# Kernel tuning notes

Hardware: AMD Instinct MI355X
Metric: run time of the kernel (lower is better)

The kernel has to match this reference:

```python
import jax, jax.numpy as jnp
import numpy as np

IN = 1    # input feature dim (hardcoded in NN)
H = 10    # LSTM hidden size (hardcoded in NN)
B = 8192  # batch
T = 256   # sequence length


def setup_inputs() -> dict:
    key = jax.random.key(0)
    ks = jax.random.split(key, 12)
    s = 0.1  # init scale for mus (mimics blitz posterior_mu_init spread)
    RHO0 = -3.0  # posterior_rho_init from the module
    return {
        "x": jax.random.normal(ks[0], (B, T, IN), jnp.float32),
        # BayesianLSTM variational parameters (blitz layout: (in, 4*H), (H, 4*H), (4*H,))
        "w_ih_mu": jax.random.normal(ks[1], (IN, 4 * H), jnp.float32) * s,
        "w_ih_rho": jnp.full((IN, 4 * H), RHO0, jnp.float32),
        "w_hh_mu": jax.random.normal(ks[2], (H, 4 * H), jnp.float32) * s,
        "w_hh_rho": jnp.full((H, 4 * H), RHO0, jnp.float32),
        "b_mu": jax.random.normal(ks[3], (4 * H,), jnp.float32) * s,
        "b_rho": jnp.full((4 * H,), RHO0, jnp.float32),
        # reparameterization noise, sampled once per forward call in blitz
        "eps_ih": jax.random.normal(ks[4], (IN, 4 * H), jnp.float32),
        "eps_hh": jax.random.normal(ks[5], (H, 4 * H), jnp.float32),
        "eps_b": jax.random.normal(ks[6], (4 * H,), jnp.float32),
        # deterministic linear head nn.Linear(10, 1)
        "lin_w": jax.random.normal(ks[7], (1, H), jnp.float32) * s,
        "lin_b": jnp.zeros((1,), jnp.float32),
    }


def reference(x, w_ih_mu, w_ih_rho, w_hh_mu, w_hh_rho, b_mu, b_rho,
              eps_ih, eps_hh, eps_b, lin_w, lin_b):
    sp = jax.nn.softplus
    # sample weights: w = mu + log1p(exp(rho)) * eps
    w_ih = w_ih_mu + sp(w_ih_rho) * eps_ih   # (IN, 4H)
    w_hh = w_hh_mu + sp(w_hh_rho) * eps_hh   # (H, 4H)
    b = b_mu + sp(b_rho) * eps_b             # (4H,)

    # precompute input contribution for all timesteps: (B, T, 4H)
    x_proj = jnp.einsum('bti,ig->btg', x, w_ih) + b

    def step(carry, xg):
        h, c = carry                      # (B, H) each
        gates = xg + h @ w_hh             # (B, 4H)
        i = jax.nn.sigmoid(gates[:, :H])
        f = jax.nn.sigmoid(gates[:, H:2 * H])
        g = jnp.tanh(gates[:, 2 * H:3 * H])
        o = jax.nn.sigmoid(gates[:, 3 * H:])
        c = f * c + i * g
        h = o * jnp.tanh(c)
        return (h, c), None

    h0 = jnp.zeros((x.shape[0], H), x.dtype)
    (h_last, _), _ = jax.lax.scan(step, (h0, h0), jnp.swapaxes(x_proj, 0, 1))
    # NN takes hidden_seq[:, -1, :] == final hidden state, then linear head
    return h_last @ lin_w.T + lin_b  # (B, 1)
```

## Files before the change

kernel.cpp:

```cpp
#include <hip/hip_runtime.h>
#include <math.h>

#define T_LEN 256
#define HID 10

typedef float v2f __attribute__((ext_vector_type(2)));

__device__ __forceinline__ v2f mk2(float a, float b) { v2f r; r.x = a; r.y = b; return r; }
__device__ __forceinline__ v2f splat2(float a) { return mk2(a, a); }

__device__ __forceinline__ float softplus_f(float x) {
    return fmaxf(x, 0.0f) + log1pf(expf(-fabsf(x)));
}
__device__ __forceinline__ float samp(const float* mu, const float* rho,
                                      const float* eps, int i) {
    return mu[i] + softplus_f(rho[i]) * eps[i];
}

__device__ __forceinline__ float fast_sigmoid(float x) {
    float e = __builtin_amdgcn_exp2f(-1.442695040888963f * x);
    return __builtin_amdgcn_rcpf(1.0f + e);
}
__device__ __forceinline__ float fast_tanh(float x) {
    float e = __builtin_amdgcn_exp2f(2.885390081777927f * x);
    return fmaf(-2.0f, __builtin_amdgcn_rcpf(e + 1.0f), 1.0f);
}

#define ROTF(hi, R) __int_as_float(__builtin_amdgcn_mov_dpp((hi), 0x120 + (R), 0xF, 0xF, true))

struct Wreg {
    v2f wsel01[16], wsel23[16];
    v2f wih01, wih23, b01, b23;
};

__device__ __forceinline__ float lstm_step(const Wreg& w, float xt, float hk,
                                           float& c)
{
    const int hi = __float_as_int(hk);
    v2f x2 = splat2(xt);
    v2f e01 = __builtin_elementwise_fma(x2, w.wih01, w.b01);
    v2f e23 = __builtin_elementwise_fma(x2, w.wih23, w.b23);
    v2f o01 = w.wsel01[0] * splat2(hk);
    v2f o23 = w.wsel23[0] * splat2(hk);
#define RSTEP(R, A01, A23)                                            \
    {                                                                 \
        v2f hr = splat2(ROTF(hi, R));                                 \
        A01 = __builtin_elementwise_fma(hr, w.wsel01[R], A01);        \
        A23 = __builtin_elementwise_fma(hr, w.wsel23[R], A23);        \
    }
    RSTEP(1,  e01, e23)
    RSTEP(2,  o01, o23)
    RSTEP(3,  e01, e23)
    RSTEP(4,  o01, o23)
    RSTEP(5,  e01, e23)
    RSTEP(6,  o01, o23)
    RSTEP(7,  e01, e23)
    RSTEP(8,  o01, o23)
    RSTEP(9,  e01, e23)
    RSTEP(10, o01, o23)
    RSTEP(11, e01, e23)
    RSTEP(12, o01, o23)
    RSTEP(13, e01, e23)
    RSTEP(14, o01, o23)
    RSTEP(15, e01, e23)
#undef RSTEP
    v2f a01 = e01 + o01;
    v2f a23 = e23 + o23;
    float ig = fast_sigmoid(a01.x);
    float fg = fast_sigmoid(a01.y);
    float gg = fast_tanh(a23.x);
    float og = fast_sigmoid(a23.y);
    c = fmaf(fg, c, ig * gg);
    return og * fast_tanh(c);
}

__global__ __launch_bounds__(64) void bayes_lstm_kernel(
    const float* __restrict__ x,
    const float* __restrict__ w_ih_mu, const float* __restrict__ w_ih_rho,
    const float* __restrict__ w_hh_mu, const float* __restrict__ w_hh_rho,
    const float* __restrict__ b_mu,    const float* __restrict__ b_rho,
    const float* __restrict__ eps_ih,  const float* __restrict__ eps_hh,
    const float* __restrict__ eps_b,
    const float* __restrict__ lin_w,   const float* __restrict__ lin_b,
    float* __restrict__ out, int n_elem)
{
    const int lane = threadIdx.x & 63;
    const int k    = lane & 15;
    const int g    = lane >> 4;
    const int b    = blockIdx.x * 4 + g;
    const int b_eff = (b < n_elem) ? b : (n_elem - 1);
    const bool un  = (k < HID);

    Wreg w;
    w.wih01 = splat2(0.f); w.wih23 = splat2(0.f);
    w.b01 = splat2(0.f);   w.b23 = splat2(0.f);
    if (un) {
        const int c0 = k, c1 = HID + k, c2 = 2 * HID + k, c3 = 3 * HID + k;
        w.wih01 = mk2(samp(w_ih_mu, w_ih_rho, eps_ih, c0), samp(w_ih_mu, w_ih_rho, eps_ih, c1));
        w.wih23 = mk2(samp(w_ih_mu, w_ih_rho, eps_ih, c2), samp(w_ih_mu, w_ih_rho, eps_ih, c3));
        w.b01   = mk2(samp(b_mu, b_rho, eps_b, c0), samp(b_mu, b_rho, eps_b, c1));
        w.b23   = mk2(samp(b_mu, b_rho, eps_b, c2), samp(b_mu, b_rho, eps_b, c3));
    }
#pragma unroll
    for (int r = 0; r < 16; ++r) {
        const int idx = (k - r) & 15;
        if (un && idx < HID) {
            const int base = idx * 4 * HID;
            w.wsel01[r] = mk2(samp(w_hh_mu, w_hh_rho, eps_hh, base + k),
                              samp(w_hh_mu, w_hh_rho, eps_hh, base + HID + k));
            w.wsel23[r] = mk2(samp(w_hh_mu, w_hh_rho, eps_hh, base + 2 * HID + k),
                              samp(w_hh_mu, w_hh_rho, eps_hh, base + 3 * HID + k));
        } else {
            w.wsel01[r] = splat2(0.f);
            w.wsel23[r] = splat2(0.f);
        }
    }

    float c = 0.f, hk = 0.f;
    const float4* xv = (const float4*)(x + (size_t)b_eff * T_LEN);
    float4 xq = xv[0];
    for (int ch = 0; ch < 64; ++ch) {
        const int nx = (ch < 63) ? ch + 1 : 63;
        float4 xn = xv[nx];
        hk = lstm_step(w, xq.x, hk, c);
        hk = lstm_step(w, xq.y, hk, c);
        hk = lstm_step(w, xq.z, hk, c);
        hk = lstm_step(w, xq.w, hk, c);
        xq = xn;
    }

    const float lw = un ? lin_w[k] : 0.f;
    float pa = hk * lw;
    pa += __shfl_xor(pa, 1, 16);
    pa += __shfl_xor(pa, 2, 16);
    pa += __shfl_xor(pa, 4, 16);
    pa += __shfl_xor(pa, 8, 16);
    if (k == 0 && b < n_elem) out[b] = pa + lin_b[0];
}

extern "C" void kernel_launch(void* const* d_in, const int* in_sizes, int n_in,
                              void* d_out, int out_size, void* d_ws, size_t ws_size,
                              hipStream_t stream) {
    const float* x        = (const float*)d_in[0];
    const float* w_ih_mu  = (const float*)d_in[1];
    const float* w_ih_rho = (const float*)d_in[2];
    const float* w_hh_mu  = (const float*)d_in[3];
    const float* w_hh_rho = (const float*)d_in[4];
    const float* b_mu     = (const float*)d_in[5];
    const float* b_rho    = (const float*)d_in[6];
    const float* eps_ih   = (const float*)d_in[7];
    const float* eps_hh   = (const float*)d_in[8];
    const float* eps_b    = (const float*)d_in[9];
    const float* lin_w    = (const float*)d_in[10];
    const float* lin_b    = (const float*)d_in[11];
    float* out = (float*)d_out;

    const int n_b = in_sizes[0] / T_LEN;
    dim3 grid((n_b + 3) / 4), block(64);
    hipLaunchKernelGGL(bayes_lstm_kernel, grid, block, 0, stream,
                       x, w_ih_mu, w_ih_rho, w_hh_mu, w_hh_rho, b_mu, b_rho,
                       eps_ih, eps_hh, eps_b, lin_w, lin_b, out, n_b);
}
```

Before: 188.1 us.

## Interleave two batch sequences per lane group and fold activation scales into weights

```diff
diff --git a/kernel.cpp b/kernel.cpp
--- a/kernel.cpp
+++ b/kernel.cpp
@@ -17,12 +17,17 @@
     return mu[i] + softplus_f(rho[i]) * eps[i];
 }
 
-__device__ __forceinline__ float fast_sigmoid(float x) {
-    float e = __builtin_amdgcn_exp2f(-1.442695040888963f * x);
-    return __builtin_amdgcn_rcpf(1.0f + e);
+#define NLOG2E (-1.442695040888963f)
+#define P2LOG2E (2.885390081777927f)
+
+__device__ __forceinline__ float sig_pre(float a) {
+    return __builtin_amdgcn_rcpf(1.0f + __builtin_amdgcn_exp2f(a));
+}
+__device__ __forceinline__ float tanh_pre(float a) {
+    return fmaf(-2.0f, __builtin_amdgcn_rcpf(__builtin_amdgcn_exp2f(a) + 1.0f), 1.0f);
 }
 __device__ __forceinline__ float fast_tanh(float x) {
-    float e = __builtin_amdgcn_exp2f(2.885390081777927f * x);
+    float e = __builtin_amdgcn_exp2f(P2LOG2E * x);
     return fmaf(-2.0f, __builtin_amdgcn_rcpf(e + 1.0f), 1.0f);
 }
 
@@ -66,10 +71,10 @@
 #undef RSTEP
     v2f a01 = e01 + o01;
     v2f a23 = e23 + o23;
-    float ig = fast_sigmoid(a01.x);
-    float fg = fast_sigmoid(a01.y);
-    float gg = fast_tanh(a23.x);
-    float og = fast_sigmoid(a23.y);
+    float ig = sig_pre(a01.x);
+    float fg = sig_pre(a01.y);
+    float gg = tanh_pre(a23.x);
+    float og = sig_pre(a23.y);
     c = fmaf(fg, c, ig * gg);
     return og * fast_tanh(c);
 }
@@ -86,56 +91,71 @@
 {
     const int lane = threadIdx.x & 63;
     const int k    = lane & 15;
-    const int g    = lane >> 4;
-    const int b    = blockIdx.x * 4 + g;
-    const int b_eff = (b < n_elem) ? b : (n_elem - 1);
+    const int row  = lane >> 4;
+    const int bA   = blockIdx.x * 8 + row * 2;
+    const int bB   = bA + 1;
+    const int bAe  = (bA < n_elem) ? bA : (n_elem - 1);
+    const int bBe  = (bB < n_elem) ? bB : (n_elem - 1);
     const bool un  = (k < HID);
 
     Wreg w;
     w.wih01 = splat2(0.f); w.wih23 = splat2(0.f);
     w.b01 = splat2(0.f);   w.b23 = splat2(0.f);
+    const v2f s01 = mk2(NLOG2E, NLOG2E);
+    const v2f s23 = mk2(P2LOG2E, NLOG2E);
     if (un) {
         const int c0 = k, c1 = HID + k, c2 = 2 * HID + k, c3 = 3 * HID + k;
-        w.wih01 = mk2(samp(w_ih_mu, w_ih_rho, eps_ih, c0), samp(w_ih_mu, w_ih_rho, eps_ih, c1));
-        w.wih23 = mk2(samp(w_ih_mu, w_ih_rho, eps_ih, c2), samp(w_ih_mu, w_ih_rho, eps_ih, c3));
-        w.b01   = mk2(samp(b_mu, b_rho, eps_b, c0), samp(b_mu, b_rho, eps_b, c1));
-        w.b23   = mk2(samp(b_mu, b_rho, eps_b, c2), samp(b_mu, b_rho, eps_b, c3));
+        w.wih01 = s01 * mk2(samp(w_ih_mu, w_ih_rho, eps_ih, c0), samp(w_ih_mu, w_ih_rho, eps_ih, c1));
+        w.wih23 = s23 * mk2(samp(w_ih_mu, w_ih_rho, eps_ih, c2), samp(w_ih_mu, w_ih_rho, eps_ih, c3));
+        w.b01   = s01 * mk2(samp(b_mu, b_rho, eps_b, c0), samp(b_mu, b_rho, eps_b, c1));
+        w.b23   = s23 * mk2(samp(b_mu, b_rho, eps_b, c2), samp(b_mu, b_rho, eps_b, c3));
     }
 #pragma unroll
     for (int r = 0; r < 16; ++r) {
         const int idx = (k - r) & 15;
         if (un && idx < HID) {
             const int base = idx * 4 * HID;
-            w.wsel01[r] = mk2(samp(w_hh_mu, w_hh_rho, eps_hh, base + k),
-                              samp(w_hh_mu, w_hh_rho, eps_hh, base + HID + k));
-            w.wsel23[r] = mk2(samp(w_hh_mu, w_hh_rho, eps_hh, base + 2 * HID + k),
-                              samp(w_hh_mu, w_hh_rho, eps_hh, base + 3 * HID + k));
+            w.wsel01[r] = s01 * mk2(samp(w_hh_mu, w_hh_rho, eps_hh, base + k),
+                                    samp(w_hh_mu, w_hh_rho, eps_hh, base + HID + k));
+            w.wsel23[r] = s23 * mk2(samp(w_hh_mu, w_hh_rho, eps_hh, base + 2 * HID + k),
+                                    samp(w_hh_mu, w_hh_rho, eps_hh, base + 3 * HID + k));
         } else {
             w.wsel01[r] = splat2(0.f);
             w.wsel23[r] = splat2(0.f);
         }
     }
 
-    float c = 0.f, hk = 0.f;
-    const float4* xv = (const float4*)(x + (size_t)b_eff * T_LEN);
-    float4 xq = xv[0];
+    float cA = 0.f, hkA = 0.f, cB = 0.f, hkB = 0.f;
+    const float4* xvA = (const float4*)(x + (size_t)bAe * T_LEN);
+    const float4* xvB = (const float4*)(x + (size_t)bBe * T_LEN);
+    float4 xqA = xvA[0], xqB = xvB[0];
     for (int ch = 0; ch < 64; ++ch) {
         const int nx = (ch < 63) ? ch + 1 : 63;
-        float4 xn = xv[nx];
-        hk = lstm_step(w, xq.x, hk, c);
-        hk = lstm_step(w, xq.y, hk, c);
-        hk = lstm_step(w, xq.z, hk, c);
-        hk = lstm_step(w, xq.w, hk, c);
-        xq = xn;
+        float4 xnA = xvA[nx];
+        float4 xnB = xvB[nx];
+        hkA = lstm_step(w, xqA.x, hkA, cA);
+        hkB = lstm_step(w, xqB.x, hkB, cB);
+        hkA = lstm_step(w, xqA.y, hkA, cA);
+        hkB = lstm_step(w, xqB.y, hkB, cB);
+        hkA = lstm_step(w, xqA.z, hkA, cA);
+        hkB = lstm_step(w, xqB.z, hkB, cB);
+        hkA = lstm_step(w, xqA.w, hkA, cA);
+        hkB = lstm_step(w, xqB.w, hkB, cB);
+        xqA = xnA; xqB = xnB;
     }
 
     const float lw = un ? lin_w[k] : 0.f;
-    float pa = hk * lw;
-    pa += __shfl_xor(pa, 1, 16);
-    pa += __shfl_xor(pa, 2, 16);
-    pa += __shfl_xor(pa, 4, 16);
-    pa += __shfl_xor(pa, 8, 16);
-    if (k == 0 && b < n_elem) out[b] = pa + lin_b[0];
+    float pa = hkA * lw;
+    float pb = hkB * lw;
+    pa += __shfl_xor(pa, 1, 16);  pb += __shfl_xor(pb, 1, 16);
+    pa += __shfl_xor(pa, 2, 16);  pb += __shfl_xor(pb, 2, 16);
+    pa += __shfl_xor(pa, 4, 16);  pb += __shfl_xor(pb, 4, 16);
+    pa += __shfl_xor(pa, 8, 16);  pb += __shfl_xor(pb, 8, 16);
+    if (k == 0) {
+        float b0 = lin_b[0];
+        if (bA < n_elem) out[bA] = pa + b0;
+        if (bB < n_elem) out[bB] = pb + b0;
+    }
 }
 
 extern "C" void kernel_launch(void* const* d_in, const int* in_sizes, int n_in,
@@ -156,7 +176,7 @@
     float* out = (float*)d_out;
 
     const int n_b = in_sizes[0] / T_LEN;
-    dim3 grid((n_b + 3) / 4), block(64);
+    dim3 grid((n_b + 7) / 8), block(64);
     hipLaunchKernelGGL(bayes_lstm_kernel, grid, block, 0, stream,
                        x, w_ih_mu, w_ih_rho, w_hh_mu, w_hh_rho, b_mu, b_rho,
                        eps_ih, eps_hh, eps_b, lin_w, lin_b, out, n_b);
```

Result: faster. 174.2 us (-7.4%).
